# Kernel optimization log

Hardware: AMD Instinct MI355X
Metric: run time of the kernel (lower is better)

Reference implementation:

```python
import jax, jax.numpy as jnp
import numpy as np

B, T, F, H, C = 128, 16, 1024, 1024, 2513


def setup_inputs() -> dict:
    key = jax.random.key(0)
    ks = jax.random.split(key, 11)
    s = 1.0 / np.sqrt(H)

    def u(k, shape):
        return jax.random.uniform(k, shape, jnp.float32, -s, s)

    return {
        "inputs": jax.random.normal(ks[0], (B, T, F), jnp.float32),
        "Wi_r": u(ks[1], (4 * H, F)),
        "Wh_r": u(ks[2], (4 * H, H)),
        "bi_r": u(ks[3], (4 * H,)),
        "bh_r": u(ks[4], (4 * H,)),
        "Wi_u": u(ks[5], (4 * H, F)),
        "Wh_u": u(ks[6], (4 * H, H)),
        "bi_u": u(ks[7], (4 * H,)),
        "bh_u": u(ks[8], (4 * H,)),
        "Wc": u(ks[9], (C, H)),
        "bc": u(ks[10], (C,)),
    }


def _lstm_gates(pre, c):
    # pre: [..., 4H] pre-activations; torch gate order i, f, g, o
    i, f, g, o = jnp.split(pre, 4, axis=-1)
    c_new = jax.nn.sigmoid(f) * c + jax.nn.sigmoid(i) * jnp.tanh(g)
    h_new = jax.nn.sigmoid(o) * jnp.tanh(c_new)
    return h_new, c_new


def reference(inputs, Wi_r, Wh_r, bi_r, bh_r, Wi_u, Wh_u, bi_u, bh_u, Wc, bc):
    # Dropout layers are identity (eval mode).
    x = inputs.transpose(1, 0, 2)  # [T, B, F]
    Tn, Bn = x.shape[0], x.shape[1]
    Hd = Wh_r.shape[1]

    # ---- rolling LSTM: collect hidden & cell at every timestep ----
    def roll_step(carry, xt):
        h, c = carry
        pre = xt @ Wi_r.T + h @ Wh_r.T + (bi_r + bh_r)
        h, c = _lstm_gates(pre, c)
        return (h, c), (h, c)

    h0 = jnp.zeros((Bn, Hd), x.dtype)
    _, (hs, cs) = jax.lax.scan(roll_step, (h0, h0), x)  # each [T, B, H]

    # ---- unrolling LSTM: for each t, feed x[t] repeated (T - t + 1) times,
    # starting from (hs[t], cs[t]); take hidden at the last step.
    # Vectorized over t: the input is constant per step, so precompute its projection.
    xi = x @ Wi_u.T + (bi_u + bh_u)  # [T, B, 4H]

    def unroll_step(carry, _):
        h, c = carry  # [T, B, H]
        pre = xi + h @ Wh_u.T
        h, c = _lstm_gates(pre, c)
        return (h, c), h

    _, hs_un = jax.lax.scan(unroll_step, (hs, cs), None, length=Tn + 1)  # [T+1, T, B, H]
    # sequence for start t has length L = T - t + 1, so last hidden is step index T - t
    idx = Tn - jnp.arange(Tn)
    h_n = hs_un[idx, jnp.arange(Tn)]  # [T, B, H]

    xcls = h_n.transpose(1, 0, 2)  # [B, T, H]
    y = xcls @ Wc.T + bc  # [B, T, num_class]
    return y
```

## Files before the change

### kernel.cpp

```cpp
#include <hip/hip_runtime.h>
#include <cstdint>

using half_t = _Float16;
using half8  = __attribute__((ext_vector_type(8))) _Float16;
using half4v = __attribute__((ext_vector_type(4))) _Float16;
using f32x4  = __attribute__((ext_vector_type(4))) float;
using flt4v  = __attribute__((ext_vector_type(4))) float;

namespace {
constexpr int kT = 16, kH = 1024, kFH = 4096, kC = 2513, kCP = 2560;
constexpr int kSlot = 128 * 1024;
constexpr int kPar  = 17 * kSlot;
}

__device__ __forceinline__ void gload16(const void* g, void* l) {
  __builtin_amdgcn_global_load_lds((const __attribute__((address_space(1))) void*)g,
                                   (__attribute__((address_space(3))) void*)l, 16, 0, 0);
}
__device__ __forceinline__ float sgm(float x) { return 1.0f / (1.0f + __expf(-x)); }

__global__ void setup_all(const flt4v* __restrict__ WiR, const flt4v* __restrict__ WhR,
                          const flt4v* __restrict__ WiU, const flt4v* __restrict__ WhU,
                          const flt4v* __restrict__ Wc, const float* __restrict__ x,
                          const float* __restrict__ biR, const float* __restrict__ bhR,
                          const float* __restrict__ biU, const float* __restrict__ bhU,
                          const float* __restrict__ bc,
                          half4v* __restrict__ WiRh, half4v* __restrict__ WhRh,
                          half4v* __restrict__ WiUh, half4v* __restrict__ WhUh,
                          half4v* __restrict__ Wch, half_t* __restrict__ xh,
                          float* __restrict__ br_p, float* __restrict__ bu_p,
                          float* __restrict__ bcp) {
  int blk = blockIdx.x;
  if (blk < 18944) {
    long i = (long)blk * 256 + threadIdx.x;
    const long Q = 1048576;
    if (i < Q) { WiRh[i] = __builtin_convertvector(WiR[i], half4v); return; }
    i -= Q;
    if (i < Q) { WhRh[i] = __builtin_convertvector(WhR[i], half4v); return; }
    i -= Q;
    if (i < Q) { WiUh[i] = __builtin_convertvector(WiU[i], half4v); return; }
    i -= Q;
    if (i < Q) { WhUh[i] = __builtin_convertvector(WhU[i], half4v); return; }
    i -= Q;
    if (i < (long)kC * kH / 4) {
      Wch[i] = __builtin_convertvector(Wc[i], half4v);
    } else if (i < (long)kCP * kH / 4) {
      half4v z = {(_Float16)0, (_Float16)0, (_Float16)0, (_Float16)0};
      Wch[i] = z;
    }
    return;
  }
  blk -= 18944;
  if (blk < 2048) {
    int t = blk >> 7, b = blk & 127;
    const flt4v* src = (const flt4v*)(x + ((long)b * kT + t) * kH);
    half4v* dst = (half4v*)(xh + (long)blk * kH);
    dst[threadIdx.x] = __builtin_convertvector(src[threadIdx.x], half4v);
    return;
  }
  blk -= 2048;
  {
    int i = blk * 256 + threadIdx.x;
    if (i < kFH) {
      int j = i >> 2, gt = i & 3;
      br_p[i] = biR[gt * kH + j] + bhR[gt * kH + j];
      bu_p[i] = biU[gt * kH + j] + bhU[gt * kH + j];
    }
    if (i < kCP) bcp[i] = (i < kC) ? bc[i] : 0.0f;
  }
}

__device__ __forceinline__ int brow_gate(int r, int j0) {
  return (((r >> 4) & 3) << 10) + j0 + ((r >> 6) << 4) + (r & 15);
}

template <int MR>
__device__ __forceinline__ void gemm_core(
    const half_t* __restrict__ A, const half_t* __restrict__ B,
    const long* ao, const long* bo, half_t* AsB, half_t* BsB,
    int tid, int wm, int wc, int row16, int g, f32x4 acc[][4]) {
  constexpr int UA = MR / 32;
  constexpr int ABUF = MR * 64;
#pragma unroll
  for (int i = 0; i < UA; ++i) gload16(A + ao[i], AsB + (i * 256 + tid) * 8);
#pragma unroll
  for (int i = 0; i < 4; ++i) gload16(B + bo[i], BsB + (i * 256 + tid) * 8);
  __syncthreads();
  int p = 0;
  for (int kt = 64; kt <= 1024; kt += 64) {
    if (kt < 1024) {
      half_t* as_n = AsB + (p ^ 1) * ABUF;
      half_t* bs_n = BsB + (p ^ 1) * 8192;
#pragma unroll
      for (int i = 0; i < UA; ++i) gload16(A + ao[i] + kt, as_n + (i * 256 + tid) * 8);
#pragma unroll
      for (int i = 0; i < 4; ++i) gload16(B + bo[i] + kt, bs_n + (i * 256 + tid) * 8);
    }
    const half_t* as_ = AsB + p * ABUF;
    const half_t* bs_ = BsB + p * 8192;
#pragma unroll
    for (int s = 0; s < 2; ++s) {
      half8 af[UA], bf[4];
#pragma unroll
      for (int a = 0; a < UA; ++a) {
        const int row = wm * (MR / 2) + (a << 4) + row16;
        const int slot = (s * 4 + g) ^ (row & 7);
        af[a] = *(const half8*)&as_[row * 64 + slot * 8];
      }
#pragma unroll
      for (int b = 0; b < 4; ++b) {
        const int row = (wc << 6) + (b << 4) + row16;
        const int slot = (s * 4 + g) ^ (row & 7);
        bf[b] = *(const half8*)&bs_[row * 64 + slot * 8];
      }
#pragma unroll
      for (int a = 0; a < UA; ++a)
#pragma unroll
        for (int b = 0; b < 4; ++b)
          acc[a][b] = __builtin_amdgcn_mfma_f32_16x16x32_f16(af[a], bf[b], acc[a][b], 0, 0, 0);
    }
    __syncthreads();
    p ^= 1;
  }
}

template <int MR>
__global__ __launch_bounds__(256, (MR == 64 ? 3 : 2)) void pipe_step(
    const int u, const int nRec, const int projBase,
    const half_t* __restrict__ xh,
    const half_t* __restrict__ WiRh, const half_t* __restrict__ WiUh,
    const float* __restrict__ brp, const float* __restrict__ bup,
    const half_t* __restrict__ Wr, const half_t* __restrict__ Wu,
    half_t* __restrict__ xiR, half_t* __restrict__ xiU,
    half_t* __restrict__ Hbuf, float* __restrict__ Cbuf) {
  __shared__ __align__(16) half_t As[2 * MR * 64];
  __shared__ __align__(16) half_t Bs[2 * 8192];
  constexpr int FA = MR / 32;
  const int tid = threadIdx.x;
  const int lane = tid & 63;
  const int w = tid >> 6, wm = w >> 1, wc = w & 1;
  const int row16 = lane & 15;
  const int g = lane >> 4;
  const int j0 = blockIdx.x << 5;
  const int sy = blockIdx.y;
  const int seg = (MR == 64) ? (sy >> 1) : sy;
  const int mrow0 = (MR == 64) ? ((sy & 1) << 6) : 0;

  f32x4 acc[FA][4];
  const f32x4 z4 = {0.f, 0.f, 0.f, 0.f};
#pragma unroll
  for (int a = 0; a < FA; ++a)
#pragma unroll
    for (int b = 0; b < 4; ++b) acc[a][b] = z4;

  int srow[4], skk[4];
#pragma unroll
  for (int i = 0; i < 4; ++i) {
    srow[i] = i * 32 + (tid >> 3);
    skk[i] = ((tid & 7) ^ (srow[i] & 7)) * 8;
  }

  if (seg < nRec) {
    const bool isRoll = (u <= 16) && (seg == 0);
    const int c = (u <= 16) ? (seg - 1) : seg;
    const int pr = (u & 1) ^ 1, pw = u & 1;
    const int slot_in = isRoll ? (u - 2) : c;
    const int slot_out = isRoll ? (u - 1) : c;
    const half_t* A  = Hbuf + (size_t)pr * kPar + (size_t)slot_in * kSlot;
    const float* Cin = Cbuf + (size_t)pr * kPar + (size_t)slot_in * kSlot;
    half_t* Ho = Hbuf + (size_t)pw * kPar + (size_t)slot_out * kSlot;
    float*  Co = Cbuf + (size_t)pw * kPar + (size_t)slot_out * kSlot;
    const half_t* W  = isRoll ? Wr : Wu;
    const half_t* xi = isRoll ? (xiR + (size_t)(u - 1) * 524288)
                              : (xiU + (size_t)c * 524288);

    long ao[FA], bo[4];
#pragma unroll
    for (int i = 0; i < FA; ++i) ao[i] = (long)(mrow0 + srow[i]) * kH + skk[i];
#pragma unroll
    for (int i = 0; i < 4; ++i) bo[i] = (long)brow_gate(srow[i], j0) * kH + skk[i];
    gemm_core<MR>(A, W, ao, bo, As, Bs, tid, wm, wc, row16, g, acc);

    const int jg = j0 + (wc << 4) + row16;
#pragma unroll
    for (int a = 0; a < FA; ++a) {
      const int mb = mrow0 + wm * (MR / 2) + (a << 4) + (g << 2);
#pragma unroll
      for (int r = 0; r < 4; ++r) {
        const int m = mb + r;
        const half4v xv = *(const half4v*)&xi[((long)m * kH + jg) * 4];
        const float pi = acc[a][0][r] + (float)xv[0];
        const float pf = acc[a][1][r] + (float)xv[1];
        const float pg = acc[a][2][r] + (float)xv[2];
        const float po = acc[a][3][r] + (float)xv[3];
        const float co = Cin[(long)m * kH + jg];
        const float cn = sgm(pf) * co + sgm(pi) * tanhf(pg);
        const float hn = sgm(po) * tanhf(cn);
        Ho[(long)m * kH + jg] = (half_t)hn;
        Co[(long)m * kH + jg] = cn;
      }
    }
  } else {
    const int p = projBase + (seg - nRec);
    int z, rr;
    if (p == 0)       { z = 0; rr = 0; }
    else if (p == 1)  { z = 1; rr = 0; }
    else if (p <= 16) { z = 0; rr = p - 1; }
    else              { z = 1; rr = p - 16; }
    const half_t* Wt = z ? WiUh : WiRh;
    const float* bias_p = z ? bup : brp;
    half_t* xi = z ? xiU : xiR;
    const int m0 = (rr << 7) + mrow0;

    long ao[FA], bo[4];
#pragma unroll
    for (int i = 0; i < FA; ++i) ao[i] = (long)(m0 + srow[i]) * kH + skk[i];
#pragma unroll
    for (int i = 0; i < 4; ++i) bo[i] = (long)brow_gate(srow[i], j0) * kH + skk[i];
    gemm_core<MR>(xh, Wt, ao, bo, As, Bs, tid, wm, wc, row16, g, acc);

    const int jg = j0 + (wc << 4) + row16;
    const f32x4 bv = *(const f32x4*)&bias_p[jg * 4];
#pragma unroll
    for (int a = 0; a < FA; ++a) {
      const int mb = m0 + wm * (MR / 2) + (a << 4) + (g << 2);
#pragma unroll
      for (int r4 = 0; r4 < 4; ++r4) {
        const float pi = acc[a][0][r4] + bv[0];
        const float pf = acc[a][1][r4] + bv[1];
        const float pg = acc[a][2][r4] + bv[2];
        const float po = acc[a][3][r4] + bv[3];
        half4v o;
        o[0] = (half_t)pi; o[1] = (half_t)pf; o[2] = (half_t)pg; o[3] = (half_t)po;
        *(half4v*)&xi[((long)(mb + r4) * kH + jg) * 4] = o;
        if (p == 0) {
          const float cn = sgm(pi) * tanhf(pg);
          const float hn = sgm(po) * tanhf(cn);
          Hbuf[(size_t)kPar + (long)(mb + r4) * kH + jg] = (half_t)hn;
          Cbuf[(size_t)kPar + (long)(mb + r4) * kH + jg] = cn;
        }
      }
    }
  }
}

__global__ __launch_bounds__(256, 3) void cls_gemm(
    const half_t* __restrict__ Hfin, const half_t* __restrict__ Wcw,
    const float* __restrict__ bcp, float* __restrict__ out) {
  __shared__ __align__(16) half_t As[2 * 4096];
  __shared__ __align__(16) half_t Bs[2 * 8192];
  const int tid = threadIdx.x;
  const int lane = tid & 63;
  const int w = tid >> 6, wm = w >> 1, wc = w & 1;
  const int row16 = lane & 15;
  const int g = lane >> 4;
  const int n00 = blockIdx.x << 7;
  const int t = blockIdx.y >> 1;
  const int m0 = (t << 7) + ((blockIdx.y & 1) << 6);

  int srow[4], skk[4];
#pragma unroll
  for (int i = 0; i < 4; ++i) {
    srow[i] = i * 32 + (tid >> 3);
    skk[i] = ((tid & 7) ^ (srow[i] & 7)) * 8;
  }
  long ao[2], bo[4];
#pragma unroll
  for (int i = 0; i < 2; ++i) ao[i] = (long)(m0 + srow[i]) * kH + skk[i];
#pragma unroll
  for (int i = 0; i < 4; ++i) bo[i] = (long)(n00 + srow[i]) * kH + skk[i];

  f32x4 acc[2][4];
  const f32x4 z4 = {0.f, 0.f, 0.f, 0.f};
#pragma unroll
  for (int a = 0; a < 2; ++a)
#pragma unroll
    for (int b = 0; b < 4; ++b) acc[a][b] = z4;

  gemm_core<64>(Hfin, Wcw, ao, bo, As, Bs, tid, wm, wc, row16, g, acc);

#pragma unroll
  for (int a = 0; a < 2; ++a) {
    const int mb = m0 + wm * 32 + (a << 4) + (g << 2);
#pragma unroll
    for (int b = 0; b < 4; ++b) {
      const int n = n00 + (wc << 6) + (b << 4) + row16;
      if (n < kC) {
        const float bvv = bcp[n];
#pragma unroll
        for (int r = 0; r < 4; ++r) {
          const int m = mb + r;
          const int bi = m & 127;
          out[((long)bi * kT + t) * kC + n] = acc[a][b][r] + bvv;
        }
      }
    }
  }
}

extern "C" void kernel_launch(void* const* d_in, const int* in_sizes, int n_in,
                              void* d_out, int out_size, void* d_ws, size_t ws_size,
                              hipStream_t stream) {
  const float* x   = (const float*)d_in[0];
  const float* WiR = (const float*)d_in[1];
  const float* WhR = (const float*)d_in[2];
  const float* biR = (const float*)d_in[3];
  const float* bhR = (const float*)d_in[4];
  const float* WiU = (const float*)d_in[5];
  const float* WhU = (const float*)d_in[6];
  const float* biU = (const float*)d_in[7];
  const float* bhU = (const float*)d_in[8];
  const float* Wc  = (const float*)d_in[9];
  const float* bc  = (const float*)d_in[10];

  size_t off = 0;
  auto alloc = [&](size_t bytes) -> void* {
    void* p = (char*)d_ws + off;
    off += (bytes + 255) & ~(size_t)255;
    return p;
  };
  half_t* xh   = (half_t*)alloc((size_t)2048 * 1024 * 2);
  half_t* WiRh = (half_t*)alloc((size_t)4096 * 1024 * 2);
  half_t* WhRh = (half_t*)alloc((size_t)4096 * 1024 * 2);
  half_t* WiUh = (half_t*)alloc((size_t)4096 * 1024 * 2);
  half_t* WhUh = (half_t*)alloc((size_t)4096 * 1024 * 2);
  half_t* Wch  = (half_t*)alloc((size_t)2560 * 1024 * 2);
  float*  br   = (float*)alloc(4096 * 4);
  float*  bu   = (float*)alloc(4096 * 4);
  float*  bcp  = (float*)alloc(2560 * 4);
  half_t* xiR  = (half_t*)alloc((size_t)2048 * 4096 * 2);
  half_t* xiU  = (half_t*)alloc((size_t)2048 * 4096 * 2);
  half_t* Hbuf = (half_t*)alloc((size_t)2 * kPar * 2);
  float*  Cbuf = (float*)alloc((size_t)2 * kPar * 4);
  float*  outp = (float*)d_out;
  (void)ws_size; (void)in_sizes; (void)n_in; (void)out_size;

  setup_all<<<21008, 256, 0, stream>>>(
      (const flt4v*)WiR, (const flt4v*)WhR, (const flt4v*)WiU, (const flt4v*)WhU,
      (const flt4v*)Wc, x, biR, bhR, biU, bhU, bc,
      (half4v*)WiRh, (half4v*)WhRh, (half4v*)WiUh, (half4v*)WhUh, (half4v*)Wch,
      xh, br, bu, bcp);

  pipe_step<64><<<dim3(32, 28), 256, 0, stream>>>(
      0, 0, 0, xh, WiRh, WiUh, br, bu, WhRh, WhUh, xiR, xiU, Hbuf, Cbuf);

  for (int u = 2; u <= 18; ++u) {
    const int nchain = (u - 2 < 15 ? u - 2 : 15) + 1;
    const int nRec = (u <= 16 ? 1 : 0) + nchain;
    int projBase = 0, nProj = 0;
    if (u == 2) { projBase = 14; nProj = 10; }
    if (u == 3) { projBase = 24; nProj = 8;  }
    if (u <= 12) {
      pipe_step<64><<<dim3(32, 2 * (nRec + nProj)), 256, 0, stream>>>(
          u, nRec, projBase, xh, WiRh, WiUh, br, bu, WhRh, WhUh, xiR, xiU,
          Hbuf, Cbuf);
    } else {
      pipe_step<128><<<dim3(32, nRec), 256, 0, stream>>>(
          u, nRec, 0, xh, WiRh, WiUh, br, bu, WhRh, WhUh, xiR, xiU,
          Hbuf, Cbuf);
    }
  }

  cls_gemm<<<dim3(20, 32), 256, 0, stream>>>(Hbuf, Wch, bcp, (float*)outp);
}
```

Measured before the change: 483.5 us.

## Overlap recurrent and classifier weight conversion with first step; rebalance projection schedule

Moves the fp16 conversion of WhR, WhU and Wc out of the setup kernel and into extra blocks of the first pipe_step launch, so the conversion overlaps with the initial input-projection GEMMs. The input projections are also spread more evenly across steps u=2..10 through a constant-memory schedule table, instead of being packed into the first few launches. This aims to shorten the serial setup phase and fill idle CUs during the early, narrow recurrence steps. The risk is extra launch-size variance, plus reliance on the first launch finishing all weight conversion before step 2 reads the converted weights, which stream ordering guarantees.

```diff
diff --git a/kernel.cpp b/kernel.cpp
--- a/kernel.cpp
+++ b/kernel.cpp
@@ -13,44 +13,36 @@
 constexpr int kPar  = 17 * kSlot;
 }
 
+__device__ __constant__ unsigned char g_seq_z[32] = {
+    0,0,1,0, 0,0,1,1, 0,0,1,1, 0,0,1,1, 0,0,1, 0,0,1, 0,0,1, 0,1,1, 1,1, 1,1};
+__device__ __constant__ unsigned char g_seq_r[32] = {
+    0,1,0,2, 3,4,1,2, 5,6,3,4, 7,8,5,6, 9,10,7, 11,12,8, 13,14,9, 15,10,11, 12,13, 14,15};
+
 __device__ __forceinline__ void gload16(const void* g, void* l) {
   __builtin_amdgcn_global_load_lds((const __attribute__((address_space(1))) void*)g,
                                    (__attribute__((address_space(3))) void*)l, 16, 0, 0);
 }
 __device__ __forceinline__ float sgm(float x) { return 1.0f / (1.0f + __expf(-x)); }
 
-__global__ void setup_all(const flt4v* __restrict__ WiR, const flt4v* __restrict__ WhR,
-                          const flt4v* __restrict__ WiU, const flt4v* __restrict__ WhU,
-                          const flt4v* __restrict__ Wc, const float* __restrict__ x,
+__global__ void setup_all(const flt4v* __restrict__ WiR, const flt4v* __restrict__ WiU,
+                          const float* __restrict__ x,
                           const float* __restrict__ biR, const float* __restrict__ bhR,
                           const float* __restrict__ biU, const float* __restrict__ bhU,
                           const float* __restrict__ bc,
-                          half4v* __restrict__ WiRh, half4v* __restrict__ WhRh,
-                          half4v* __restrict__ WiUh, half4v* __restrict__ WhUh,
-                          half4v* __restrict__ Wch, half_t* __restrict__ xh,
+                          half4v* __restrict__ WiRh, half4v* __restrict__ WiUh,
+                          half_t* __restrict__ xh,
                           float* __restrict__ br_p, float* __restrict__ bu_p,
                           float* __restrict__ bcp) {
   int blk = blockIdx.x;
-  if (blk < 18944) {
+  if (blk < 8192) {
     long i = (long)blk * 256 + threadIdx.x;
     const long Q = 1048576;
     if (i < Q) { WiRh[i] = __builtin_convertvector(WiR[i], half4v); return; }
     i -= Q;
-    if (i < Q) { WhRh[i] = __builtin_convertvector(WhR[i], half4v); return; }
-    i -= Q;
-    if (i < Q) { WiUh[i] = __builtin_convertvector(WiU[i], half4v); return; }
-    i -= Q;
-    if (i < Q) { WhUh[i] = __builtin_convertvector(WhU[i], half4v); return; }
-    i -= Q;
-    if (i < (long)kC * kH / 4) {
-      Wch[i] = __builtin_convertvector(Wc[i], half4v);
-    } else if (i < (long)kCP * kH / 4) {
-      half4v z = {(_Float16)0, (_Float16)0, (_Float16)0, (_Float16)0};
-      Wch[i] = z;
-    }
+    WiUh[i] = __builtin_convertvector(WiU[i], half4v);
     return;
   }
-  blk -= 18944;
+  blk -= 8192;
   if (blk < 2048) {
     int t = blk >> 7, b = blk & 127;
     const flt4v* src = (const flt4v*)(x + ((long)b * kT + t) * kH);
@@ -126,13 +118,17 @@
 
 template <int MR>
 __global__ __launch_bounds__(256, (MR == 64 ? 3 : 2)) void pipe_step(
-    const int u, const int nRec, const int projBase,
+    const int u, const int nRec, const int projStart, const int nProj,
     const half_t* __restrict__ xh,
     const half_t* __restrict__ WiRh, const half_t* __restrict__ WiUh,
     const float* __restrict__ brp, const float* __restrict__ bup,
     const half_t* __restrict__ Wr, const half_t* __restrict__ Wu,
     half_t* __restrict__ xiR, half_t* __restrict__ xiU,
-    half_t* __restrict__ Hbuf, float* __restrict__ Cbuf) {
+    half_t* __restrict__ Hbuf, float* __restrict__ Cbuf,
+    const flt4v* __restrict__ WhRf, const flt4v* __restrict__ WhUf,
+    const flt4v* __restrict__ Wcf,
+    half4v* __restrict__ WhRhD, half4v* __restrict__ WhUhD,
+    half4v* __restrict__ WchD) {
   __shared__ __align__(16) half_t As[2 * MR * 64];
   __shared__ __align__(16) half_t Bs[2 * 8192];
   constexpr int FA = MR / 32;
@@ -145,6 +141,26 @@
   const int sy = blockIdx.y;
   const int seg = (MR == 64) ? (sy >> 1) : sy;
   const int mrow0 = (MR == 64) ? ((sy & 1) << 6) : 0;
+  const int nTot = nRec + nProj;
+
+  if (MR == 64 && sy >= 2 * nTot) {
+    const long TCB = (long)(gridDim.y - 2 * nTot) * 32;
+    const long fc = (long)(sy - 2 * nTot) * 32 + blockIdx.x;
+    const long Q = 1048576, total = 2 * Q + (long)kCP * kH / 4;
+    const half4v z4h = {(_Float16)0, (_Float16)0, (_Float16)0, (_Float16)0};
+    for (long i = fc * 256 + tid; i < total; i += TCB * 256) {
+      if (i < Q) {
+        WhRhD[i] = __builtin_convertvector(WhRf[i], half4v);
+      } else if (i < 2 * Q) {
+        WhUhD[i - Q] = __builtin_convertvector(WhUf[i - Q], half4v);
+      } else {
+        const long k = i - 2 * Q;
+        WchD[k] = (k < (long)kC * kH / 4)
+                      ? __builtin_convertvector(Wcf[k], half4v) : z4h;
+      }
+    }
+    return;
+  }
 
   f32x4 acc[FA][4];
   const f32x4 z4 = {0.f, 0.f, 0.f, 0.f};
@@ -201,12 +217,9 @@
       }
     }
   } else {
-    const int p = projBase + (seg - nRec);
-    int z, rr;
-    if (p == 0)       { z = 0; rr = 0; }
-    else if (p == 1)  { z = 1; rr = 0; }
-    else if (p <= 16) { z = 0; rr = p - 1; }
-    else              { z = 1; rr = p - 16; }
+    const int s = projStart + (seg - nRec);
+    const int z = g_seq_z[s];
+    const int rr = g_seq_r[s];
     const half_t* Wt = z ? WiUh : WiRh;
     const float* bias_p = z ? bup : brp;
     half_t* xi = z ? xiU : xiR;
@@ -233,7 +246,7 @@
         half4v o;
         o[0] = (half_t)pi; o[1] = (half_t)pf; o[2] = (half_t)pg; o[3] = (half_t)po;
         *(half4v*)&xi[((long)(mb + r4) * kH + jg) * 4] = o;
-        if (p == 0) {
+        if (s == 0) {
           const float cn = sgm(pi) * tanhf(pg);
           const float hn = sgm(po) * tanhf(cn);
           Hbuf[(size_t)kPar + (long)(mb + r4) * kH + jg] = (half_t)hn;
@@ -335,29 +348,31 @@
   float*  outp = (float*)d_out;
   (void)ws_size; (void)in_sizes; (void)n_in; (void)out_size;
 
-  setup_all<<<21008, 256, 0, stream>>>(
-      (const flt4v*)WiR, (const flt4v*)WhR, (const flt4v*)WiU, (const flt4v*)WhU,
-      (const flt4v*)Wc, x, biR, bhR, biU, bhU, bc,
-      (half4v*)WiRh, (half4v*)WhRh, (half4v*)WiUh, (half4v*)WhUh, (half4v*)Wch,
-      xh, br, bu, bcp);
-
-  pipe_step<64><<<dim3(32, 28), 256, 0, stream>>>(
-      0, 0, 0, xh, WiRh, WiUh, br, bu, WhRh, WhUh, xiR, xiU, Hbuf, Cbuf);
-
+  setup_all<<<10256, 256, 0, stream>>>(
+      (const flt4v*)WiR, (const flt4v*)WiU, x, biR, bhR, biU, bhU, bc,
+      (half4v*)WiRh, (half4v*)WiUh, xh, br, bu, bcp);
+
+  pipe_step<64><<<dim3(32, 2 * 4 + 16), 256, 0, stream>>>(
+      0, 0, 0, 4, xh, WiRh, WiUh, br, bu, WhRh, WhUh, xiR, xiU, Hbuf, Cbuf,
+      (const flt4v*)WhR, (const flt4v*)WhU, (const flt4v*)Wc,
+      (half4v*)WhRh, (half4v*)WhUh, (half4v*)Wch);
+
+  static const int pjs[19] = {0,0, 4, 8, 12, 16, 19, 22, 25, 28, 30, 0,0,0,0,0,0,0,0};
+  static const int pjn[19] = {0,0, 4, 4,  4,  3,  3,  3,  3,  2,  2, 0,0,0,0,0,0,0,0};
   for (int u = 2; u <= 18; ++u) {
     const int nchain = (u - 2 < 15 ? u - 2 : 15) + 1;
     const int nRec = (u <= 16 ? 1 : 0) + nchain;
-    int projBase = 0, nProj = 0;
-    if (u == 2) { projBase = 14; nProj = 10; }
-    if (u == 3) { projBase = 24; nProj = 8;  }
+    const int nProj = pjn[u];
     if (u <= 12) {
       pipe_step<64><<<dim3(32, 2 * (nRec + nProj)), 256, 0, stream>>>(
-          u, nRec, projBase, xh, WiRh, WiUh, br, bu, WhRh, WhUh, xiR, xiU,
-          Hbuf, Cbuf);
+          u, nRec, pjs[u], nProj, xh, WiRh, WiUh, br, bu, WhRh, WhUh, xiR, xiU,
+          Hbuf, Cbuf, (const flt4v*)WhR, (const flt4v*)WhU, (const flt4v*)Wc,
+          (half4v*)WhRh, (half4v*)WhUh, (half4v*)Wch);
     } else {
       pipe_step<128><<<dim3(32, nRec), 256, 0, stream>>>(
-          u, nRec, 0, xh, WiRh, WiUh, br, bu, WhRh, WhUh, xiR, xiU,
-          Hbuf, Cbuf);
+          u, nRec, 0, 0, xh, WiRh, WiUh, br, bu, WhRh, WhUh, xiR, xiU,
+          Hbuf, Cbuf, (const flt4v*)WhR, (const flt4v*)WhU, (const flt4v*)Wc,
+          (half4v*)WhRh, (half4v*)WhUh, (half4v*)Wch);
     }
   }
 
```

Measured after the change: 475.3 us. No clear change (-1.7%).

## Rebalance input-projection schedule across steps and speed up LSTM gate math

Applied to the files above, without the earlier changes.

The input-projection tiles are no longer front-loaded into the first launches. A constant lookup table now spreads them across recurrent steps 2 through 8, so each step runs a few projection tiles alongside the small recurrent GEMMs, which is meant to fill idle CUs on the dependent chain. The gate epilogue now uses hardware reciprocal and an exp-based tanh instead of tanhf, and it loads the xi and c values before the GEMM so their latency is hidden. The faster activations lose a little precision, and the new ordering must still produce each projection before its consumer step.

```diff
diff --git a/kernel.cpp b/kernel.cpp
--- a/kernel.cpp
+++ b/kernel.cpp
@@ -13,11 +13,21 @@
 constexpr int kPar  = 17 * kSlot;
 }
 
+__device__ __constant__ unsigned char g_seq_z[32] = {
+    0,0,1,0, 0,0,1,1, 0,0,1,1, 0,0,1,1, 0,0,1, 0,0,1, 0,0,1, 0,1,1, 1,1, 1,1};
+__device__ __constant__ unsigned char g_seq_r[32] = {
+    0,1,0,2, 3,4,1,2, 5,6,3,4, 7,8,5,6, 9,10,7, 11,12,8, 13,14,9, 15,10,11, 12,13, 14,15};
+
 __device__ __forceinline__ void gload16(const void* g, void* l) {
   __builtin_amdgcn_global_load_lds((const __attribute__((address_space(1))) void*)g,
                                    (__attribute__((address_space(3))) void*)l, 16, 0, 0);
 }
-__device__ __forceinline__ float sgm(float x) { return 1.0f / (1.0f + __expf(-x)); }
+__device__ __forceinline__ float sgm(float x) {
+  return __builtin_amdgcn_rcpf(1.0f + __expf(-x));
+}
+__device__ __forceinline__ float ftanh(float x) {
+  return 1.0f - 2.0f * __builtin_amdgcn_rcpf(1.0f + __expf(2.0f * x));
+}
 
 __global__ void setup_all(const flt4v* __restrict__ WiR, const flt4v* __restrict__ WhR,
                           const flt4v* __restrict__ WiU, const flt4v* __restrict__ WhU,
@@ -126,7 +136,7 @@
 
 template <int MR>
 __global__ __launch_bounds__(256, (MR == 64 ? 3 : 2)) void pipe_step(
-    const int u, const int nRec, const int projBase,
+    const int u, const int nRec, const int projStart,
     const half_t* __restrict__ xh,
     const half_t* __restrict__ WiRh, const half_t* __restrict__ WiUh,
     const float* __restrict__ brp, const float* __restrict__ bup,
@@ -174,6 +184,20 @@
     const half_t* xi = isRoll ? (xiR + (size_t)(u - 1) * 524288)
                               : (xiU + (size_t)c * 524288);
 
+    const int jg = j0 + (wc << 4) + row16;
+    float cpre[FA][4];
+    half4v xpre[FA][4];
+#pragma unroll
+    for (int a = 0; a < FA; ++a) {
+      const int mb = mrow0 + wm * (MR / 2) + (a << 4) + (g << 2);
+#pragma unroll
+      for (int r = 0; r < 4; ++r) {
+        const long idx = (long)(mb + r) * kH + jg;
+        xpre[a][r] = *(const half4v*)&xi[idx * 4];
+        cpre[a][r] = Cin[idx];
+      }
+    }
+
     long ao[FA], bo[4];
 #pragma unroll
     for (int i = 0; i < FA; ++i) ao[i] = (long)(mrow0 + srow[i]) * kH + skk[i];
@@ -181,37 +205,35 @@
     for (int i = 0; i < 4; ++i) bo[i] = (long)brow_gate(srow[i], j0) * kH + skk[i];
     gemm_core<MR>(A, W, ao, bo, As, Bs, tid, wm, wc, row16, g, acc);
 
-    const int jg = j0 + (wc << 4) + row16;
 #pragma unroll
     for (int a = 0; a < FA; ++a) {
       const int mb = mrow0 + wm * (MR / 2) + (a << 4) + (g << 2);
 #pragma unroll
       for (int r = 0; r < 4; ++r) {
         const int m = mb + r;
-        const half4v xv = *(const half4v*)&xi[((long)m * kH + jg) * 4];
+        const half4v xv = xpre[a][r];
         const float pi = acc[a][0][r] + (float)xv[0];
         const float pf = acc[a][1][r] + (float)xv[1];
         const float pg = acc[a][2][r] + (float)xv[2];
         const float po = acc[a][3][r] + (float)xv[3];
-        const float co = Cin[(long)m * kH + jg];
-        const float cn = sgm(pf) * co + sgm(pi) * tanhf(pg);
-        const float hn = sgm(po) * tanhf(cn);
+        const float cn = sgm(pf) * cpre[a][r] + sgm(pi) * ftanh(pg);
+        const float hn = sgm(po) * ftanh(cn);
         Ho[(long)m * kH + jg] = (half_t)hn;
         Co[(long)m * kH + jg] = cn;
       }
     }
   } else {
-    const int p = projBase + (seg - nRec);
-    int z, rr;
-    if (p == 0)       { z = 0; rr = 0; }
-    else if (p == 1)  { z = 1; rr = 0; }
-    else if (p <= 16) { z = 0; rr = p - 1; }
-    else              { z = 1; rr = p - 16; }
+    const int s = projStart + (seg - nRec);
+    const int z = g_seq_z[s];
+    const int rr = g_seq_r[s];
     const half_t* Wt = z ? WiUh : WiRh;
     const float* bias_p = z ? bup : brp;
     half_t* xi = z ? xiU : xiR;
     const int m0 = (rr << 7) + mrow0;
 
+    const int jg = j0 + (wc << 4) + row16;
+    const f32x4 bv = *(const f32x4*)&bias_p[jg * 4];
+
     long ao[FA], bo[4];
 #pragma unroll
     for (int i = 0; i < FA; ++i) ao[i] = (long)(m0 + srow[i]) * kH + skk[i];
@@ -219,8 +241,6 @@
     for (int i = 0; i < 4; ++i) bo[i] = (long)brow_gate(srow[i], j0) * kH + skk[i];
     gemm_core<MR>(xh, Wt, ao, bo, As, Bs, tid, wm, wc, row16, g, acc);
 
-    const int jg = j0 + (wc << 4) + row16;
-    const f32x4 bv = *(const f32x4*)&bias_p[jg * 4];
 #pragma unroll
     for (int a = 0; a < FA; ++a) {
       const int mb = m0 + wm * (MR / 2) + (a << 4) + (g << 2);
@@ -233,9 +253,9 @@
         half4v o;
         o[0] = (half_t)pi; o[1] = (half_t)pf; o[2] = (half_t)pg; o[3] = (half_t)po;
         *(half4v*)&xi[((long)(mb + r4) * kH + jg) * 4] = o;
-        if (p == 0) {
-          const float cn = sgm(pi) * tanhf(pg);
-          const float hn = sgm(po) * tanhf(cn);
+        if (s == 0) {
+          const float cn = sgm(pi) * ftanh(pg);
+          const float hn = sgm(po) * ftanh(cn);
           Hbuf[(size_t)kPar + (long)(mb + r4) * kH + jg] = (half_t)hn;
           Cbuf[(size_t)kPar + (long)(mb + r4) * kH + jg] = cn;
         }
@@ -258,6 +278,11 @@
   const int t = blockIdx.y >> 1;
   const int m0 = (t << 7) + ((blockIdx.y & 1) << 6);
 
+  float bpre[4];
+#pragma unroll
+  for (int b = 0; b < 4; ++b)
+    bpre[b] = bcp[n00 + (wc << 6) + (b << 4) + row16];
+
   int srow[4], skk[4];
 #pragma unroll
   for (int i = 0; i < 4; ++i) {
@@ -286,12 +311,11 @@
     for (int b = 0; b < 4; ++b) {
       const int n = n00 + (wc << 6) + (b << 4) + row16;
       if (n < kC) {
-        const float bvv = bcp[n];
 #pragma unroll
         for (int r = 0; r < 4; ++r) {
           const int m = mb + r;
           const int bi = m & 127;
-          out[((long)bi * kT + t) * kC + n] = acc[a][b][r] + bvv;
+          out[((long)bi * kT + t) * kC + n] = acc[a][b][r] + bpre[b];
         }
       }
     }
@@ -341,18 +365,18 @@
       (half4v*)WiRh, (half4v*)WhRh, (half4v*)WiUh, (half4v*)WhUh, (half4v*)Wch,
       xh, br, bu, bcp);
 
-  pipe_step<64><<<dim3(32, 28), 256, 0, stream>>>(
+  pipe_step<64><<<dim3(32, 24), 256, 0, stream>>>(
       0, 0, 0, xh, WiRh, WiUh, br, bu, WhRh, WhUh, xiR, xiU, Hbuf, Cbuf);
 
+  static const int pjs[19] = {0,0, 12, 15, 18, 21, 24, 27, 30, 0,0,0,0,0,0,0,0,0,0};
+  static const int pjn[19] = {0,0,  3,  3,  3,  3,  3,  3,  2, 0,0,0,0,0,0,0,0,0,0};
   for (int u = 2; u <= 18; ++u) {
     const int nchain = (u - 2 < 15 ? u - 2 : 15) + 1;
     const int nRec = (u <= 16 ? 1 : 0) + nchain;
-    int projBase = 0, nProj = 0;
-    if (u == 2) { projBase = 14; nProj = 10; }
-    if (u == 3) { projBase = 24; nProj = 8;  }
+    const int nProj = pjn[u];
     if (u <= 12) {
       pipe_step<64><<<dim3(32, 2 * (nRec + nProj)), 256, 0, stream>>>(
-          u, nRec, projBase, xh, WiRh, WiUh, br, bu, WhRh, WhUh, xiR, xiU,
+          u, nRec, pjs[u], xh, WiRh, WiUh, br, bu, WhRh, WhUh, xiR, xiU,
           Hbuf, Cbuf);
     } else {
       pipe_step<128><<<dim3(32, nRec), 256, 0, stream>>>(
```

Measured after the change: 432.8 us. 10.5% less time.
